# Kernel tuning notes

Hardware: AMD Instinct MI355X
Metric: run time of the kernel (lower is better)

Reference implementation:

```python
import jax, jax.numpy as jnp
import numpy as np

K = 64
PI = np.float32(np.pi)


def setup_inputs() -> dict:
    key = jax.random.key(0)
    k1, k2 = jax.random.split(key)
    B, N = 4096, 21
    rotation = jax.random.normal(k1, (B, N, 3, 3), dtype=jnp.float32)
    conditions = jax.random.normal(k2, (B, N, 4 * K), dtype=jnp.float32)
    permute = np.arange(3).astype(np.int64)  # static permutation indices
    return {"rotation": rotation, "conditions": conditions, "permute": permute}


def _mobius_forward(rotation, conditions, p0, p1, p2):
    B, N = rotation.shape[0], rotation.shape[1]
    I3 = jnp.eye(3, dtype=rotation.dtype)

    x = rotation[..., p0]  # [B,N,3]
    y = rotation[..., p1]  # [B,N,3]

    # compute_mcl_parameters_nd
    weights = conditions[..., :K]                      # [B,N,K]
    w = conditions[..., K:].reshape(B, N, K, 3)        # [B,N,K,3]
    proj = I3 - jnp.einsum('bni,bnj->bnij', y, y)      # [B,N,3,3]
    w = jnp.einsum('bnij,bnkj->bnki', proj, w)
    r = -x
    r = r / jnp.linalg.norm(r, axis=-1, keepdims=True)
    v = jnp.cross(y, r)
    v = v / jnp.linalg.norm(v, axis=-1, keepdims=True)
    weights = jax.nn.softplus(weights)
    weights = weights / jnp.sum(weights, axis=-1, keepdims=True)
    w_norm = jnp.linalg.norm(w, axis=-1, keepdims=True)
    w = 0.7 / (1.0 + w_norm) * w

    # _forward_nd
    z = x
    zw = z[:, :, None, :] - w                          # [B,N,K,3]
    zw_norm = jnp.linalg.norm(zw, axis=-1)             # [B,N,K]
    w_norm2 = jnp.sum(w * w, axis=-1)                  # [B,N,K]
    h_z = ((1.0 - w_norm2) / zw_norm ** 2)[..., None] * zw - w  # [B,N,K,3]

    radians = jnp.arctan2(jnp.einsum('bnki,bni->bnk', h_z, v),
                          jnp.einsum('bnki,bni->bnk', h_z, r))
    ang = jnp.where(radians >= 0, radians, radians + 2.0 * PI)
    ang = jnp.sum(weights * ang, axis=2, keepdims=True)          # [B,N,1]
    tx = r * jnp.cos(ang) + v * jnp.sin(ang)                     # [B,N,3]

    zw_unit = zw / zw_norm[..., None]
    theta = jnp.arctan2(jnp.einsum('bni,bni->bn', x, v),
                        jnp.einsum('bni,bni->bn', x, r))[..., None]  # [B,N,1]
    dz_dtheta = -jnp.sin(theta) * r + jnp.cos(theta) * v             # [B,N,3]
    dh_dz = (1.0 - w_norm2)[..., None, None] * (
        I3 - 2.0 * jnp.einsum('bnki,bnkj->bnkij', zw_unit, zw_unit)
    ) / (zw_norm ** 2)[..., None, None]                              # [B,N,K,3,3]
    dh_dtheta = jnp.einsum('bnkpq,bnq->bnkp', dh_dz, dz_dtheta)      # [B,N,K,3]
    dtx = jnp.sum(jnp.linalg.norm(dh_dtheta, axis=-1) * weights, axis=2)  # [B,N]
    ldj = jnp.log(dtx)

    if (p1 - p0 == 1) or (p1 - p0 == -2):
        tz = jnp.cross(tx, y)
    else:
        tz = jnp.cross(y, tx)
    tz = tz / jnp.linalg.norm(tz, axis=-1, keepdims=True)

    cols = [None, None, None]
    cols[p0] = tx
    cols[p1] = y
    cols[p2] = tz
    trotation = jnp.stack(cols, axis=-1)  # [B,N,3,3]
    return trotation, jnp.sum(ldj, axis=-1)


def reference(rotation, conditions, permute):
    p0, p1, p2 = int(permute[0]), int(permute[1]), int(permute[2])
    return _mobius_forward(rotation, conditions, p0, p1, p2)
```

## Files before the change

### kernel.cpp

```cpp
#include <hip/hip_runtime.h>
#include <math.h>

#define PI_F    3.14159265358979323846f
#define TWO_PI  6.28318530717958647692f
#define HALF_PI 1.57079632679489661923f

__device__ __forceinline__ float frcp(float x)  { return __builtin_amdgcn_rcpf(x); }
__device__ __forceinline__ float frsq(float x)  { return __builtin_amdgcn_rsqf(x); }
__device__ __forceinline__ float fsqrt(float x) { return __builtin_amdgcn_sqrtf(x); }

__device__ __forceinline__ float fast_atan2_2pi(float y, float x) {
    float ax = fabsf(x), ay = fabsf(y);
    float mx = fmaxf(ax, ay), mn = fminf(ax, ay);
    float a  = (mx > 0.0f) ? mn * frcp(mx) : 0.0f;
    float s  = a * a;
    float r  = fmaf(s, fmaf(s, fmaf(s, fmaf(s, 0.0208351f, -0.085133f),
                                    0.180141f), -0.3302995f), 0.9998660f) * a;
    if (ay > ax) r = HALF_PI - r;
    if (x < 0.0f) r = PI_F - r;
    return (y < 0.0f) ? (TWO_PI - r) : r;
}

__global__ __launch_bounds__(448)
void mobius_fwd(const float* __restrict__ rot,
                const float* __restrict__ cond,
                const void* __restrict__ perm,
                float* __restrict__ out,
                int B, int N)
{
    const int wave = threadIdx.x >> 6;
    const int lane = threadIdx.x & 63;
    const int sub  = lane >> 4;
    const int j    = lane & 15;
    const int nwav = blockDim.x >> 6;

    const int b0     = blockIdx.x * 4;
    const int nb     = min(4, B - b0);
    const int nit    = N * nb;
    const int nquads = (nit + 3) >> 2;

    const int* pi = (const int*)perm;
    int p0 = pi[0], p1 = pi[1], p2 = pi[2];
    bool pok = ((unsigned)p0 < 3u) && ((unsigned)p1 < 3u) && ((unsigned)p2 < 3u)
               && (p0 != p1) && (p0 != p2) && (p1 != p2);
    if (!pok) {
        const long long* pl = (const long long*)perm;
        p0 = (int)pl[0]; p1 = (int)pl[1]; p2 = (int)pl[2];
    }

    __shared__ float s_ldj[256];

    const size_t base_item = (size_t)b0 * N;

    for (int q = wave; q < nquads; q += nwav) {
        const int  i0    = 4 * q + sub;
        const bool valid = (i0 < nit);
        const int  iv    = valid ? i0 : 0;
        const size_t item = base_item + iv;

        const float* R = rot + item * 9;
        float x0 = R[p0], x1 = R[3 + p0], x2 = R[6 + p0];
        float y0 = R[p1], y1 = R[3 + p1], y2 = R[6 + p1];

        float inv_xn = frsq(x0 * x0 + x1 * x1 + x2 * x2);
        float r0 = -x0 * inv_xn, r1 = -x1 * inv_xn, r2 = -x2 * inv_xn;

        float v0 = y1 * r2 - y2 * r1;
        float v1 = y2 * r0 - y0 * r2;
        float v2 = y0 * r1 - y1 * r0;
        float inv_vn = frsq(v0 * v0 + v1 * v1 + v2 * v2);
        v0 *= inv_vn; v1 *= inv_vn; v2 *= inv_vn;

        const float* C = cond + item * 256;
        float4 pw4 = *(const float4*)(C + 4 * j);
        float4 fa  = *(const float4*)(C + 64 + 12 * j);
        float4 fb  = *(const float4*)(C + 68 + 12 * j);
        float4 fc  = *(const float4*)(C + 72 + 12 * j);

        float pp = 0.0f, pa = 0.0f, pd = 0.0f;

        auto docomp = [&](float pw, float w0, float w1, float w2) {
            float yd = y0 * w0 + y1 * w1 + y2 * w2;
            w0 -= y0 * yd; w1 -= y1 * yd; w2 -= y2 * yd;
            float qn  = w0 * w0 + w1 * w1 + w2 * w2;
            float sc = 0.7f * frcp(1.0f + fsqrt(qn));
            w0 *= sc; w1 *= sc; w2 *= sc;
            float wn2 = w0 * w0 + w1 * w1 + w2 * w2;
            float zw0 = x0 - w0, zw1 = x1 - w1, zw2 = x2 - w2;
            float zwn2 = zw0 * zw0 + zw1 * zw1 + zw2 * zw2;
            float c = (1.0f - wn2) * frcp(zwn2);
            float h0 = c * zw0 - w0, h1 = c * zw1 - w1, h2 = c * zw2 - w2;
            float hv = h0 * v0 + h1 * v1 + h2 * v2;
            float hr = h0 * r0 + h1 * r1 + h2 * r2;
            float ang = fast_atan2_2pi(hv, hr);
            float t = __expf(-fabsf(pw));
            float p = fmaxf(pw, 0.0f) + __logf(1.0f + t);
            pp += p; pa += p * ang; pd += p * c;
        };
        docomp(pw4.x, fa.x, fa.y, fa.z);
        docomp(pw4.y, fa.w, fb.x, fb.y);
        docomp(pw4.z, fb.z, fb.w, fc.x);
        docomp(pw4.w, fc.y, fc.z, fc.w);

        #pragma unroll
        for (int off = 8; off >= 1; off >>= 1) {
            pp += __shfl_xor(pp, off, 64);
            pa += __shfl_xor(pa, off, 64);
            pd += __shfl_xor(pd, off, 64);
        }

        if (j == 0 && valid) {
            float ip   = frcp(pp);
            float angT = pa * ip;
            float ldj  = __logf(pd * ip);

            float sa, ca;
            __sincosf(angT, &sa, &ca);
            float t0 = r0 * ca + v0 * sa;
            float t1 = r1 * ca + v1 * sa;
            float t2 = r2 * ca + v2 * sa;

            float u0, u1, u2;
            int dd = p1 - p0;
            if (dd == 1 || dd == -2) {
                u0 = t1 * y2 - t2 * y1;
                u1 = t2 * y0 - t0 * y2;
                u2 = t0 * y1 - t1 * y0;
            } else {
                u0 = y1 * t2 - y2 * t1;
                u1 = y2 * t0 - y0 * t2;
                u2 = y0 * t1 - y1 * t0;
            }
            float iun = frsq(u0 * u0 + u1 * u1 + u2 * u2);
            u0 *= iun; u1 *= iun; u2 *= iun;

            float* T = out + item * 9;
            T[p0] = t0; T[3 + p0] = t1; T[6 + p0] = t2;
            T[p1] = y0; T[3 + p1] = y1; T[6 + p1] = y2;
            T[p2] = u0; T[3 + p2] = u1; T[6 + p2] = u2;

            s_ldj[i0] = ldj;
        }
    }

    __syncthreads();
    if (threadIdx.x < nb) {
        float acc = 0.0f;
        for (int n = 0; n < N; ++n) acc += s_ldj[threadIdx.x * N + n];
        out[(size_t)B * N * 9 + b0 + threadIdx.x] = acc;
    }
}

extern "C" void kernel_launch(void* const* d_in, const int* in_sizes, int n_in,
                              void* d_out, int out_size, void* d_ws, size_t ws_size,
                              hipStream_t stream) {
    const float* rot  = (const float*)d_in[0];
    const float* cond = (const float*)d_in[1];
    const void*  perm = d_in[2];
    float* out = (float*)d_out;

    int items = in_sizes[0] / 9;
    int B = out_size - items * 9;
    int N = items / B;

    int grid = (B + 3) / 4;
    mobius_fwd<<<dim3(grid), dim3(448), 0, stream>>>(rot, cond, perm, out, B, N);
}
```

Before: 25.37 us.

## Stage conditions through LDS with coalesced loads, simplify per-component math, parallelize stores

Each wave now loads four items' condition rows with fully coalesced float4 loads per lane and stages them through shared memory. Lanes then read their strided weight triples from LDS instead of issuing scattered global loads. The per-component maths is rewritten algebraically with dot products (projection norm, z-w norm and h components) so the projected w and h vectors are never built, and softplus uses log(1+exp). The 3x3 output is written by nine lanes in parallel instead of one lane doing nine scalar stores. This adds LDS traffic and more shared-memory use, and the unguarded softplus form can overflow for large inputs.

New measurement: 26.55 us. 1.05x slower.

```diff
diff --git a/kernel.cpp b/kernel.cpp
--- a/kernel.cpp
+++ b/kernel.cpp
@@ -47,12 +47,27 @@
         const long long* pl = (const long long*)perm;
         p0 = (int)pl[0]; p1 = (int)pl[1]; p2 = (int)pl[2];
     }
+    const int dd = p1 - p0;
+    const bool swapc = (dd == 1 || dd == -2);
 
+    __shared__ __align__(16) float smem[7][4][264];
     __shared__ float s_ldj[256];
 
     const size_t base_item = (size_t)b0 * N;
 
     for (int q = wave; q < nquads; q += nwav) {
+        float4 stg0, stg1, stg2, stg3;
+        {
+            int s0i = min(4 * q + 0, nit - 1);
+            int s1i = min(4 * q + 1, nit - 1);
+            int s2i = min(4 * q + 2, nit - 1);
+            int s3i = min(4 * q + 3, nit - 1);
+            stg0 = ((const float4*)(cond + (base_item + s0i) * 256))[lane];
+            stg1 = ((const float4*)(cond + (base_item + s1i) * 256))[lane];
+            stg2 = ((const float4*)(cond + (base_item + s2i) * 256))[lane];
+            stg3 = ((const float4*)(cond + (base_item + s3i) * 256))[lane];
+        }
+
         const int  i0    = 4 * q + sub;
         const bool valid = (i0 < nit);
         const int  iv    = valid ? i0 : 0;
@@ -62,45 +77,56 @@
         float x0 = R[p0], x1 = R[3 + p0], x2 = R[6 + p0];
         float y0 = R[p1], y1 = R[3 + p1], y2 = R[6 + p1];
 
-        float inv_xn = frsq(x0 * x0 + x1 * x1 + x2 * x2);
-        float r0 = -x0 * inv_xn, r1 = -x1 * inv_xn, r2 = -x2 * inv_xn;
+        float xn2    = x0 * x0 + x1 * x1 + x2 * x2;
+        float inv_xn = frsq(xn2);
+        float xn     = xn2 * inv_xn;
+        float xy     = x0 * y0 + x1 * y1 + x2 * y2;
+        float yn2    = y0 * y0 + y1 * y1 + y2 * y2;
+        float negA   = yn2 - 2.0f;
 
-        float v0 = y1 * r2 - y2 * r1;
-        float v1 = y2 * r0 - y0 * r2;
-        float v2 = y0 * r1 - y1 * r0;
-        float inv_vn = frsq(v0 * v0 + v1 * v1 + v2 * v2);
-        v0 *= inv_vn; v1 *= inv_vn; v2 *= inv_vn;
+        float cv0 = x1 * y2 - x2 * y1;
+        float cv1 = x2 * y0 - x0 * y2;
+        float cv2 = x0 * y1 - x1 * y0;
+        float inv_cn = frsq(cv0 * cv0 + cv1 * cv1 + cv2 * cv2);
+        float v0 = cv0 * inv_cn, v1 = cv1 * inv_cn, v2 = cv2 * inv_cn;
 
-        const float* C = cond + item * 256;
-        float4 pw4 = *(const float4*)(C + 4 * j);
-        float4 fa  = *(const float4*)(C + 64 + 12 * j);
-        float4 fb  = *(const float4*)(C + 68 + 12 * j);
-        float4 fc  = *(const float4*)(C + 72 + 12 * j);
+        *(float4*)&smem[wave][0][4 * lane] = stg0;
+        *(float4*)&smem[wave][1][4 * lane] = stg1;
+        *(float4*)&smem[wave][2][4 * lane] = stg2;
+        *(float4*)&smem[wave][3][4 * lane] = stg3;
+
+        const float* myl = &smem[wave][sub][0];
+        float4 pw4 = *(const float4*)(myl + 4 * j);
+        float4 fa  = *(const float4*)(myl + 64 + 12 * j);
+        float4 fb  = *(const float4*)(myl + 68 + 12 * j);
+        float4 fc  = *(const float4*)(myl + 72 + 12 * j);
+
+        float PW[4] = {pw4.x, pw4.y, pw4.z, pw4.w};
+        float W0[4] = {fa.x, fa.w, fb.z, fc.y};
+        float W1[4] = {fa.y, fb.x, fb.w, fc.z};
+        float W2[4] = {fa.z, fb.y, fc.x, fc.w};
 
         float pp = 0.0f, pa = 0.0f, pd = 0.0f;
-
-        auto docomp = [&](float pw, float w0, float w1, float w2) {
-            float yd = y0 * w0 + y1 * w1 + y2 * w2;
-            w0 -= y0 * yd; w1 -= y1 * yd; w2 -= y2 * yd;
-            float qn  = w0 * w0 + w1 * w1 + w2 * w2;
-            float sc = 0.7f * frcp(1.0f + fsqrt(qn));
-            w0 *= sc; w1 *= sc; w2 *= sc;
-            float wn2 = w0 * w0 + w1 * w1 + w2 * w2;
-            float zw0 = x0 - w0, zw1 = x1 - w1, zw2 = x2 - w2;
-            float zwn2 = zw0 * zw0 + zw1 * zw1 + zw2 * zw2;
-            float c = (1.0f - wn2) * frcp(zwn2);
-            float h0 = c * zw0 - w0, h1 = c * zw1 - w1, h2 = c * zw2 - w2;
-            float hv = h0 * v0 + h1 * v1 + h2 * v2;
-            float hr = h0 * r0 + h1 * r1 + h2 * r2;
+        #pragma unroll
+        for (int cc = 0; cc < 4; ++cc) {
+            float w0 = W0[cc], w1 = W1[cc], w2 = W2[cc];
+            float yw  = y0 * w0 + y1 * w1 + y2 * w2;
+            float wp2 = w0 * w0 + w1 * w1 + w2 * w2;
+            float xwp = x0 * w0 + x1 * w1 + x2 * w2;
+            float vwp = v0 * w0 + v1 * w1 + v2 * w2;
+            float qn  = fmaxf(fmaf(yw * yw, negA, wp2), 0.0f);
+            float sc  = 0.7f * frcp(1.0f + fsqrt(qn));
+            float wn2 = (sc * sc) * qn;
+            float xw  = sc * fmaf(-xy, yw, xwp);
+            float zwn2 = fmaf(-2.0f, xw, xn2 + wn2);
+            float c   = (1.0f - wn2) * frcp(zwn2);
+            float cp1 = c + 1.0f;
+            float hv  = -(cp1 * (sc * vwp));
+            float hr  = fmaf(cp1, xw * inv_xn, -(c * xn));
             float ang = fast_atan2_2pi(hv, hr);
-            float t = __expf(-fabsf(pw));
-            float p = fmaxf(pw, 0.0f) + __logf(1.0f + t);
-            pp += p; pa += p * ang; pd += p * c;
-        };
-        docomp(pw4.x, fa.x, fa.y, fa.z);
-        docomp(pw4.y, fa.w, fb.x, fb.y);
-        docomp(pw4.z, fb.z, fb.w, fc.x);
-        docomp(pw4.w, fc.y, fc.z, fc.w);
+            float p   = __logf(1.0f + __expf(PW[cc]));
+            pp += p; pa = fmaf(p, ang, pa); pd = fmaf(p, c, pd);
+        }
 
         #pragma unroll
         for (int off = 8; off >= 1; off >>= 1) {
@@ -109,37 +135,41 @@
             pd += __shfl_xor(pd, off, 64);
         }
 
-        if (j == 0 && valid) {
-            float ip   = frcp(pp);
-            float angT = pa * ip;
-            float ldj  = __logf(pd * ip);
+        float ip   = frcp(pp);
+        float angT = pa * ip;
+        float ldj  = __logf(pd * ip);
 
-            float sa, ca;
-            __sincosf(angT, &sa, &ca);
-            float t0 = r0 * ca + v0 * sa;
-            float t1 = r1 * ca + v1 * sa;
-            float t2 = r2 * ca + v2 * sa;
+        float sa, ca;
+        __sincosf(angT, &sa, &ca);
+        float r0 = -x0 * inv_xn, r1 = -x1 * inv_xn, r2 = -x2 * inv_xn;
+        float t0 = fmaf(r0, ca, v0 * sa);
+        float t1 = fmaf(r1, ca, v1 * sa);
+        float t2 = fmaf(r2, ca, v2 * sa);
 
-            float u0, u1, u2;
-            int dd = p1 - p0;
-            if (dd == 1 || dd == -2) {
-                u0 = t1 * y2 - t2 * y1;
-                u1 = t2 * y0 - t0 * y2;
-                u2 = t0 * y1 - t1 * y0;
-            } else {
-                u0 = y1 * t2 - y2 * t1;
-                u1 = y2 * t0 - y0 * t2;
-                u2 = y0 * t1 - y1 * t0;
+        float u0, u1, u2;
+        if (swapc) {
+            u0 = t1 * y2 - t2 * y1;
+            u1 = t2 * y0 - t0 * y2;
+            u2 = t0 * y1 - t1 * y0;
+        } else {
+            u0 = y1 * t2 - y2 * t1;
+            u1 = y2 * t0 - y0 * t2;
+            u2 = y0 * t1 - y1 * t0;
+        }
+        float iun = frsq(u0 * u0 + u1 * u1 + u2 * u2);
+        u0 *= iun; u1 *= iun; u2 *= iun;
+
+        if (valid) {
+            if (j < 9) {
+                int row = (j >= 6) ? 2 : (j >= 3) ? 1 : 0;
+                int cp  = j - 3 * row;
+                float tr = (row == 0) ? t0 : (row == 1) ? t1 : t2;
+                float yr = (row == 0) ? y0 : (row == 1) ? y1 : y2;
+                float ur = (row == 0) ? u0 : (row == 1) ? u1 : u2;
+                float val = (cp == p0) ? tr : (cp == p1) ? yr : ur;
+                out[item * 9 + j] = val;
             }
-            float iun = frsq(u0 * u0 + u1 * u1 + u2 * u2);
-            u0 *= iun; u1 *= iun; u2 *= iun;
-
-            float* T = out + item * 9;
-            T[p0] = t0; T[3 + p0] = t1; T[6 + p0] = t2;
-            T[p1] = y0; T[3 + p1] = y1; T[6 + p1] = y2;
-            T[p2] = u0; T[3 + p2] = u1; T[6 + p2] = u2;
-
-            s_ldj[i0] = ldj;
+            if (j == 0) s_ldj[i0] = ldj;
         }
     }
 
```
